# Kernel optimization log

Measured on AMD Instinct MI355X. Metric: run time of the kernel, lower is better.

The kernel has to match this reference:

```python
import jax, jax.numpy as jnp
import numpy as np

D_IN = 1024
D_OUT = 1024
SEQ = 4096


def setup_inputs() -> dict:
    key = jax.random.key(0)
    kx, kq, kk, kv = jax.random.split(key, 4)
    s = 1.0 / np.sqrt(D_IN)
    return {
        "x": jax.random.normal(kx, (SEQ, D_IN), dtype=jnp.float32),
        # torch Linear weights: shape [d_out, d_in], y = x @ W.T
        "Wq": jax.random.uniform(kq, (D_OUT, D_IN), jnp.float32, -s, s),
        "Wk": jax.random.uniform(kk, (D_OUT, D_IN), jnp.float32, -s, s),
        "Wv": jax.random.uniform(kv, (D_OUT, D_IN), jnp.float32, -s, s),
    }


def reference(x, Wq, Wk, Wv):
    # QKV projections (no bias)
    q = x @ Wq.T  # [N, d_out]
    k = x @ Wk.T
    v = x @ Wv.T
    scale = 1.0 / jnp.sqrt(jnp.asarray(k.shape[-1], x.dtype))
    att = jax.nn.softmax((q @ k.T) * scale, axis=-1)  # [N, N]
    return att @ v  # [N, d_out]
```

## Files before the change

### kernel.cpp

```cpp
#include <hip/hip_runtime.h>
#include <hip/hip_bf16.h>
#include <math.h>

typedef __attribute__((ext_vector_type(8))) short short8;
typedef __attribute__((ext_vector_type(4))) float floatx4;

static __device__ __forceinline__ unsigned short f2bf(float f) {
    union { float f; unsigned int u; } a; a.f = f;
    unsigned int u = a.u;
    return (unsigned short)((u + 0x7FFFu + ((u >> 16) & 1u)) >> 16);
}

static __device__ __forceinline__ void cvt8(const float* __restrict__ src,
                                            unsigned short* __restrict__ dst, int i) {
    float4 v0 = *(const float4*)(src + i);
    float4 v1 = *(const float4*)(src + i + 4);
    ushort4 o0, o1;
    o0.x = f2bf(v0.x); o0.y = f2bf(v0.y); o0.z = f2bf(v0.z); o0.w = f2bf(v0.w);
    o1.x = f2bf(v1.x); o1.y = f2bf(v1.y); o1.z = f2bf(v1.z); o1.w = f2bf(v1.w);
    *(ushort4*)(dst + i) = o0;
    *(ushort4*)(dst + i + 4) = o1;
}

__global__ __launch_bounds__(256)
void cvt_x_zero(const float* __restrict__ src, unsigned short* __restrict__ dst,
                int n, float* __restrict__ l) {
    if ((int)blockIdx.x == gridDim.x - 1) {
        float4 z = {0.f, 0.f, 0.f, 0.f};
        #pragma unroll
        for (int c = 0; c < 4; c++)
            *(float4*)(l + threadIdx.x * 16 + c * 4) = z;
        return;
    }
    int i = (blockIdx.x * 256 + threadIdx.x) * 8;
    if (i < n) cvt8(src, dst, i);
}

struct W3 { const float* s[3]; unsigned short* d[3]; };
__global__ __launch_bounds__(256)
void cvt_w3(W3 a, int n) {
    int i = (blockIdx.x * 256 + threadIdx.x) * 8;
    if (i < n) cvt8(a.s[blockIdx.z], a.d[blockIdx.z], i);
}

template<int BM, int BN, int BK, int TI, int TJ, int WCOLS>
__device__ __forceinline__ void gemm_core(const unsigned short* __restrict__ A,
                                          const unsigned short* __restrict__ B,
                                          int lda, int k_begin, int k_end,
                                          unsigned short* sA, unsigned short* sB,
                                          floatx4 (&acc)[TI][TJ],
                                          int bm, int bn)
{
    constexpr int CPR = BK / 8;
    constexpr int RPR = 2048 / BK;
    const int t    = threadIdx.x;
    const int wave = t >> 6;
    const int lane = t & 63;
    const int wm = (wave / WCOLS) * (TI * 16);
    const int wn = (wave % WCOLS) * (TJ * 16);

    const int srow   = t / CPR;
    const int schunk = t % CPR;
    const int gchunk = schunk ^ (srow & (CPR - 1));
    const int lm  = lane & 15;
    const int swz = lm & (CPR - 1);

    for (int k0 = k_begin; k0 < k_end; k0 += BK) {
        __syncthreads();
        #pragma unroll
        for (int r = 0; r < (BM * BK) / 2048; r++) {
            const unsigned short* gA =
                A + (size_t)(bm + srow + r * RPR) * lda + k0 + gchunk * 8;
            __builtin_amdgcn_global_load_lds(
                (const __attribute__((address_space(1))) void*)gA,
                (__attribute__((address_space(3))) void*)((char*)sA + wave * 1024 + r * 4096),
                16, 0, 0);
        }
        #pragma unroll
        for (int r = 0; r < (BN * BK) / 2048; r++) {
            const unsigned short* gB =
                B + (size_t)(bn + srow + r * RPR) * lda + k0 + gchunk * 8;
            __builtin_amdgcn_global_load_lds(
                (const __attribute__((address_space(1))) void*)gB,
                (__attribute__((address_space(3))) void*)((char*)sB + wave * 1024 + r * 4096),
                16, 0, 0);
        }
        __syncthreads();

        #pragma unroll
        for (int kk = 0; kk < BK; kk += 32) {
            const int c  = (kk >> 3) + (lane >> 4);
            const int ce = ((c ^ swz) << 3);
            short8 a_frag[TI], b_frag[TJ];
            #pragma unroll
            for (int i = 0; i < TI; i++)
                a_frag[i] = *(const short8*)&sA[(wm + i * 16 + lm) * BK + ce];
            #pragma unroll
            for (int j = 0; j < TJ; j++)
                b_frag[j] = *(const short8*)&sB[(wn + j * 16 + lm) * BK + ce];
            #pragma unroll
            for (int i = 0; i < TI; i++)
                #pragma unroll
                for (int j = 0; j < TJ; j++)
                    acc[i][j] = __builtin_amdgcn_mfma_f32_16x16x32_bf16(
                        a_frag[i], b_frag[j], acc[i][j], 0, 0, 0);
        }
    }
}


struct P3 { const unsigned short* W[3]; unsigned short* O[3]; };
__global__ __launch_bounds__(256)
void proj3(const unsigned short* __restrict__ xb, P3 a) {
    __shared__ unsigned short sA[64 * 64];
    __shared__ unsigned short sB[128 * 64];
    const int z = blockIdx.z;
    const unsigned short* B = a.W[z];
    unsigned short* O = a.O[z];
    const bool trans = (z == 2);
    const int ldc = trans ? 4096 : 1024;
    const float scale = (z == 0) ? 0.03125f : 1.0f;

    floatx4 acc[4][2];
    #pragma unroll
    for (int i = 0; i < 4; i++)
        #pragma unroll
        for (int j = 0; j < 2; j++) { floatx4 zz = {0.f,0.f,0.f,0.f}; acc[i][j] = zz; }

    const int bm = blockIdx.y * 64, bn = blockIdx.x * 128;
    gemm_core<64, 128, 64, 4, 2, 4>(xb, B, 1024, 0, 1024, sA, sB, acc, bm, bn);

    const int lane = threadIdx.x & 63, wave = threadIdx.x >> 6;
    const int wn = (wave & 3) * 32;
    const int lm = lane & 15, rq = (lane >> 4) * 4;
    #pragma unroll
    for (int i = 0; i < 4; i++)
        #pragma unroll
        for (int j = 0; j < 2; j++) {
            int tm = bm + i * 16 + rq;
            int tn = bn + wn + j * 16 + lm;
            #pragma unroll
            for (int r = 0; r < 4; r++) {
                unsigned short h = f2bf(acc[i][j][r] * scale);
                size_t idx = trans ? ((size_t)tn * ldc + (tm + r))
                                   : ((size_t)(tm + r) * ldc + tn);
                O[idx] = h;
            }
        }
}

__global__ __launch_bounds__(256)
void gemm_ps(const unsigned short* __restrict__ q, const unsigned short* __restrict__ k,
             unsigned short* __restrict__ Pm, float* __restrict__ l) {
    __shared__ unsigned short sA[128 * 128];
    __shared__ unsigned short sB[128 * 128];

    const int lid = blockIdx.x;
    const int xcd = lid & 7;
    const int i8  = lid >> 3;
    const int by  = (xcd & 1) * 16 + (i8 & 15);
    const int bx  = (xcd >> 1) * 8 + (i8 >> 4);

    floatx4 acc[4][4];
    #pragma unroll
    for (int i = 0; i < 4; i++)
        #pragma unroll
        for (int j = 0; j < 4; j++) { floatx4 zz = {0.f,0.f,0.f,0.f}; acc[i][j] = zz; }

    const int bm = by * 128, bn = bx * 128;
    gemm_core<128, 128, 128, 4, 4, 2>(q, k, 1024, 0, 1024, sA, sB, acc, bm, bn);

    const int lane = threadIdx.x & 63, wave = threadIdx.x >> 6;
    const int wm = (wave >> 1) * 64, wn = (wave & 1) * 64;
    const int lm = lane & 15, rq = (lane >> 4) * 4;
    #pragma unroll
    for (int i = 0; i < 4; i++) {
        #pragma unroll
        for (int r = 0; r < 4; r++) {
            int row = bm + wm + i * 16 + rq + r;
            float rs = 0.f;
            #pragma unroll
            for (int j = 0; j < 4; j++) {
                float e = __expf(acc[i][j][r]);
                rs += e;
                int tn = bn + wn + j * 16 + lm;
                Pm[(size_t)row * 4096 + tn] = f2bf(e);
            }
            rs += __shfl_xor(rs, 1);
            rs += __shfl_xor(rs, 2);
            rs += __shfl_xor(rs, 4);
            rs += __shfl_xor(rs, 8);
            if (lm == 0) atomicAdd(l + row, rs);
        }
    }
}

__global__ __launch_bounds__(256)
void gemm_o(const unsigned short* __restrict__ Pm, const unsigned short* __restrict__ vT,
            const float* __restrict__ l, float* __restrict__ out) {
    __shared__ unsigned short sA[64 * 128];
    __shared__ unsigned short sB[128 * 128];

    const int lid = blockIdx.x;
    const int r8  = lid & 7;
    const int w64 = lid & 63;
    const int c   = w64 >> 3;
    const int row = (lid >> 6) * 8 + r8;

    floatx4 acc[4][2];
    #pragma unroll
    for (int i = 0; i < 4; i++)
        #pragma unroll
        for (int j = 0; j < 2; j++) { floatx4 zz = {0.f,0.f,0.f,0.f}; acc[i][j] = zz; }

    const int bm = row * 64, bn = c * 128;
    gemm_core<64, 128, 128, 4, 2, 4>(Pm, vT, 4096, 0, 4096, sA, sB, acc, bm, bn);

    const int lane = threadIdx.x & 63, wave = threadIdx.x >> 6;
    const int wn = (wave & 3) * 32;
    const int lm = lane & 15, rq = (lane >> 4) * 4;
    #pragma unroll
    for (int i = 0; i < 4; i++) {
        int tm = bm + i * 16 + rq;
        float inv[4];
        #pragma unroll
        for (int r = 0; r < 4; r++) inv[r] = 1.0f / l[tm + r];
        #pragma unroll
        for (int j = 0; j < 2; j++) {
            int tn = bn + wn + j * 16 + lm;
            #pragma unroll
            for (int r = 0; r < 4; r++)
                out[(size_t)(tm + r) * 1024 + tn] = acc[i][j][r] * inv[r];
        }
    }
}

extern "C" void kernel_launch(void* const* d_in, const int* in_sizes, int n_in,
                              void* d_out, int out_size, void* d_ws, size_t ws_size,
                              hipStream_t stream) {
    const float* x  = (const float*)d_in[0];
    const float* Wq = (const float*)d_in[1];
    const float* Wk = (const float*)d_in[2];
    const float* Wv = (const float*)d_in[3];
    float* out = (float*)d_out;

    const int SEQ = 4096, D = 1024;
    char* ws = (char*)d_ws;
    const size_t MB = 1u << 20;
    unsigned short* vTb = (unsigned short*)(ws);
    unsigned short* xb  = (unsigned short*)(ws + 8 * MB);
    unsigned short* Wqb = (unsigned short*)(ws + 16 * MB);
    unsigned short* Wkb = (unsigned short*)(ws + 18 * MB);
    unsigned short* Wvb = (unsigned short*)(ws + 20 * MB);
    unsigned short* qb  = (unsigned short*)(ws + 22 * MB);
    unsigned short* kb  = (unsigned short*)(ws + 30 * MB);
    unsigned short* P   = (unsigned short*)(ws + 38 * MB);
    float*          l   = (float*)(ws + 70 * MB);

    dim3 blk(256);
    cvt_x_zero<<<(SEQ * D) / 2048 + 1, blk, 0, stream>>>(x, xb, SEQ * D, l);
    W3 w3 = {{Wq, Wk, Wv}, {Wqb, Wkb, Wvb}};
    cvt_w3<<<dim3((D * D) / 2048, 1, 3), blk, 0, stream>>>(w3, D * D);

    P3 p3 = {{Wqb, Wkb, Wvb}, {qb, kb, vTb}};
    proj3<<<dim3(D / 128, SEQ / 64, 3), blk, 0, stream>>>(xb, p3);

    gemm_ps<<<dim3(1024), blk, 0, stream>>>(qb, kb, P, l);

    gemm_o<<<dim3(512), blk, 0, stream>>>(P, vTb, l, out);
}
```

Baseline: 227.4 us.

## Merge conversion kernels, enlarge projection tiles, load P directly to registers in output GEMM

Folds the x and weight bf16 conversions plus the zeroing of l into one launch to cut launch overhead. The projection GEMM moves from 64x128 to 128x128 tiles with 2x2 waves, which raises reuse per block but halves the grid. The output GEMM stops staging P through shared memory and has each wave load its A fragments straight from global memory. Only vT goes through swizzled LDS via direct global-to-LDS loads, trading LDS traffic and sync work for more global load pressure.

```diff
diff --git a/kernel.cpp b/kernel.cpp
--- a/kernel.cpp
+++ b/kernel.cpp
@@ -22,25 +22,23 @@
     *(ushort4*)(dst + i + 4) = o1;
 }
 
+struct CV { const float* x; unsigned short* xb;
+            const float* W[3]; unsigned short* Wb[3]; float* l; };
 __global__ __launch_bounds__(256)
-void cvt_x_zero(const float* __restrict__ src, unsigned short* __restrict__ dst,
-                int n, float* __restrict__ l) {
-    if ((int)blockIdx.x == gridDim.x - 1) {
-        float4 z = {0.f, 0.f, 0.f, 0.f};
+void cvt_all(CV a) {
+    int b = blockIdx.x, t = threadIdx.x;
+    if (b < 2048) {
+        cvt8(a.x, a.xb, (b * 256 + t) * 8);
+    } else if (b < 3584) {
+        int z  = (b - 2048) >> 9;
+        int bb = (b - 2048) & 511;
+        cvt8(a.W[z], a.Wb[z], (bb * 256 + t) * 8);
+    } else {
+        float4 zz = {0.f, 0.f, 0.f, 0.f};
         #pragma unroll
         for (int c = 0; c < 4; c++)
-            *(float4*)(l + threadIdx.x * 16 + c * 4) = z;
-        return;
-    }
-    int i = (blockIdx.x * 256 + threadIdx.x) * 8;
-    if (i < n) cvt8(src, dst, i);
-}
-
-struct W3 { const float* s[3]; unsigned short* d[3]; };
-__global__ __launch_bounds__(256)
-void cvt_w3(W3 a, int n) {
-    int i = (blockIdx.x * 256 + threadIdx.x) * 8;
-    if (i < n) cvt8(a.s[blockIdx.z], a.d[blockIdx.z], i);
+            *(float4*)(a.l + t * 16 + c * 4) = zz;
+    }
 }
 
 template<int BM, int BN, int BK, int TI, int TJ, int WCOLS>
@@ -112,7 +110,7 @@
 struct P3 { const unsigned short* W[3]; unsigned short* O[3]; };
 __global__ __launch_bounds__(256)
 void proj3(const unsigned short* __restrict__ xb, P3 a) {
-    __shared__ unsigned short sA[64 * 64];
+    __shared__ unsigned short sA[128 * 64];
     __shared__ unsigned short sB[128 * 64];
     const int z = blockIdx.z;
     const unsigned short* B = a.W[z];
@@ -121,23 +119,23 @@
     const int ldc = trans ? 4096 : 1024;
     const float scale = (z == 0) ? 0.03125f : 1.0f;
 
-    floatx4 acc[4][2];
+    floatx4 acc[4][4];
     #pragma unroll
     for (int i = 0; i < 4; i++)
         #pragma unroll
-        for (int j = 0; j < 2; j++) { floatx4 zz = {0.f,0.f,0.f,0.f}; acc[i][j] = zz; }
-
-    const int bm = blockIdx.y * 64, bn = blockIdx.x * 128;
-    gemm_core<64, 128, 64, 4, 2, 4>(xb, B, 1024, 0, 1024, sA, sB, acc, bm, bn);
+        for (int j = 0; j < 4; j++) { floatx4 zz = {0.f,0.f,0.f,0.f}; acc[i][j] = zz; }
+
+    const int bm = blockIdx.y * 128, bn = blockIdx.x * 128;
+    gemm_core<128, 128, 64, 4, 4, 2>(xb, B, 1024, 0, 1024, sA, sB, acc, bm, bn);
 
     const int lane = threadIdx.x & 63, wave = threadIdx.x >> 6;
-    const int wn = (wave & 3) * 32;
+    const int wm = (wave >> 1) * 64, wn = (wave & 1) * 64;
     const int lm = lane & 15, rq = (lane >> 4) * 4;
     #pragma unroll
     for (int i = 0; i < 4; i++)
         #pragma unroll
-        for (int j = 0; j < 2; j++) {
-            int tm = bm + i * 16 + rq;
+        for (int j = 0; j < 4; j++) {
+            int tm = bm + wm + i * 16 + rq;
             int tn = bn + wn + j * 16 + lm;
             #pragma unroll
             for (int r = 0; r < 4; r++) {
@@ -198,7 +196,6 @@
 __global__ __launch_bounds__(256)
 void gemm_o(const unsigned short* __restrict__ Pm, const unsigned short* __restrict__ vT,
             const float* __restrict__ l, float* __restrict__ out) {
-    __shared__ unsigned short sA[64 * 128];
     __shared__ unsigned short sB[128 * 128];
 
     const int lid = blockIdx.x;
@@ -207,18 +204,62 @@
     const int c   = w64 >> 3;
     const int row = (lid >> 6) * 8 + r8;
 
+    const int t = threadIdx.x, wave = t >> 6, lane = t & 63;
+    const int bm = row * 64, bn = c * 128;
+    const int wn = (wave & 3) * 32;
+
+    const int srow   = t >> 4;
+    const int schunk = t & 15;
+    const int gchunk = schunk ^ (srow & 15);
+    const int lm = lane & 15, quad = lane >> 4;
+    const int swz = lm & 15;
+
     floatx4 acc[4][2];
     #pragma unroll
     for (int i = 0; i < 4; i++)
         #pragma unroll
         for (int j = 0; j < 2; j++) { floatx4 zz = {0.f,0.f,0.f,0.f}; acc[i][j] = zz; }
 
-    const int bm = row * 64, bn = c * 128;
-    gemm_core<64, 128, 128, 4, 2, 4>(Pm, vT, 4096, 0, 4096, sA, sB, acc, bm, bn);
-
-    const int lane = threadIdx.x & 63, wave = threadIdx.x >> 6;
-    const int wn = (wave & 3) * 32;
-    const int lm = lane & 15, rq = (lane >> 4) * 4;
+    const unsigned short* aBase = Pm + (size_t)(bm + lm) * 4096 + quad * 8;
+
+    for (int k0 = 0; k0 < 4096; k0 += 128) {
+        __syncthreads();
+        #pragma unroll
+        for (int r = 0; r < 8; r++) {
+            const unsigned short* gB =
+                vT + (size_t)(bn + srow + r * 16) * 4096 + k0 + gchunk * 8;
+            __builtin_amdgcn_global_load_lds(
+                (const __attribute__((address_space(1))) void*)gB,
+                (__attribute__((address_space(3))) void*)((char*)sB + wave * 1024 + r * 4096),
+                16, 0, 0);
+        }
+        short8 a_frag[4][4];
+        #pragma unroll
+        for (int kk = 0; kk < 4; kk++)
+            #pragma unroll
+            for (int i = 0; i < 4; i++)
+                a_frag[kk][i] = *(const short8*)(aBase + (size_t)i * 16 * 4096
+                                                 + k0 + kk * 32);
+        __syncthreads();
+
+        #pragma unroll
+        for (int kk = 0; kk < 4; kk++) {
+            const int cc = kk * 4 + quad;
+            const int ce = ((cc ^ swz) << 3);
+            short8 b_frag[2];
+            #pragma unroll
+            for (int j = 0; j < 2; j++)
+                b_frag[j] = *(const short8*)&sB[(wn + j * 16 + lm) * 128 + ce];
+            #pragma unroll
+            for (int i = 0; i < 4; i++)
+                #pragma unroll
+                for (int j = 0; j < 2; j++)
+                    acc[i][j] = __builtin_amdgcn_mfma_f32_16x16x32_bf16(
+                        a_frag[kk][i], b_frag[j], acc[i][j], 0, 0, 0);
+        }
+    }
+
+    const int rq = quad * 4;
     #pragma unroll
     for (int i = 0; i < 4; i++) {
         int tm = bm + i * 16 + rq;
@@ -258,12 +299,11 @@
     float*          l   = (float*)(ws + 70 * MB);
 
     dim3 blk(256);
-    cvt_x_zero<<<(SEQ * D) / 2048 + 1, blk, 0, stream>>>(x, xb, SEQ * D, l);
-    W3 w3 = {{Wq, Wk, Wv}, {Wqb, Wkb, Wvb}};
-    cvt_w3<<<dim3((D * D) / 2048, 1, 3), blk, 0, stream>>>(w3, D * D);
+    CV cv = {x, xb, {Wq, Wk, Wv}, {Wqb, Wkb, Wvb}, l};
+    cvt_all<<<dim3(3585), blk, 0, stream>>>(cv);
 
     P3 p3 = {{Wqb, Wkb, Wvb}, {qb, kb, vTb}};
-    proj3<<<dim3(D / 128, SEQ / 64, 3), blk, 0, stream>>>(xb, p3);
+    proj3<<<dim3(D / 128, SEQ / 128, 3), blk, 0, stream>>>(xb, p3);
 
     gemm_ps<<<dim3(1024), blk, 0, stream>>>(qb, kb, P, l);
 
```

Measured after the change: 321.9 us. 41.5% more time.
